# Optimization experiments

Hardware: AMD Instinct MI355X
Metric: run time of the kernel (lower is better)

Reference implementation:

```python
import jax, jax.numpy as jnp
import numpy as np

N_NODES = 20000   # len(set(idx_i)); edge targets cover all nodes
N_EDGES = 320000
F = 128           # feature dim f
N_RBF = 20        # n radial basis functions
R_CUT = 5.0


def setup_inputs() -> dict:
    key = jax.random.key(0)
    ks = jax.random.split(key, 8)
    s = jax.random.normal(ks[0], (N_EDGES, 1, F), dtype=jnp.float32)
    r = jax.random.normal(ks[1], (N_EDGES, 3), dtype=jnp.float32)
    v = jax.random.normal(ks[2], (N_EDGES, 3, F), dtype=jnp.float32)
    idx_i = jax.random.randint(ks[3], (N_EDGES,), 0, N_NODES, dtype=jnp.int32)
    W_phi = jax.random.normal(ks[4], (F, 3 * F), dtype=jnp.float32) * 0.05
    b_phi = jnp.zeros((3 * F,), dtype=jnp.float32)
    W_w = jax.random.normal(ks[5], (N_RBF, 3 * F), dtype=jnp.float32) * 0.05
    b_w = jnp.zeros((3 * F,), dtype=jnp.float32)
    return {"s": s, "r": r, "v": v, "idx_i": idx_i,
            "W_phi": W_phi, "b_phi": b_phi, "W_w": W_w, "b_w": b_w}


def reference(s, r, v, idx_i, W_phi, b_phi, W_w, b_w):
    # phi network: [E,1,F] -> [E,1,3F]
    phi_out = jnp.einsum('eif,fg->eig', s, W_phi) + b_phi

    # RBF on edge vector norms: [E,1,1] -> [E,1,n]
    r_norm = jnp.linalg.norm(r, axis=1, keepdims=True)[:, :, None]  # [E,1,1]
    n_vals = jnp.arange(1, N_RBF + 1, dtype=jnp.float32)            # [n]
    rbf = jnp.sin(n_vals * (jnp.pi / R_CUT) * r_norm) / r_norm      # [E,1,n]
    # cosine cutoff applied to rbf values (faithful to source)
    rbf = jnp.where(rbf <= R_CUT,
                    0.5 * (jnp.cos(jnp.pi * rbf / R_CUT) + 1.0),
                    jnp.zeros_like(rbf))

    # w network: [E,1,n] -> [E,1,3F]
    w = jnp.einsum('ein,ng->eig', rbf, W_w) + b_w

    split = w * phi_out                    # [E,1,3F]
    sp0 = split[..., :F]                   # gates v
    sp1 = split[..., F:2 * F]              # scalar message
    sp2 = split[..., 2 * F:]               # gates direction

    # scatter-add scalar messages -> [N,1,F]
    out_s = jax.ops.segment_sum(sp1, idx_i, num_segments=N_NODES)

    # direction term: detached r, normalized by GLOBAL Frobenius norm (faithful)
    org_r = jax.lax.stop_gradient(r)
    org_r = org_r / jnp.linalg.norm(org_r)         # [E,3]
    dir_msg = sp2 * org_r[:, :, None]              # [E,3,F]
    v_msg = dir_msg + sp0 * v                      # [E,3,F]

    # scatter-add vector messages -> [N,3,F]
    out_v = jax.ops.segment_sum(v_msg, idx_i, num_segments=N_NODES)
    return out_v, out_s
```

## Files before the change

kernel.cpp:

```cpp
#include <hip/hip_runtime.h>
#include <hip/hip_bf16.h>
#include <math.h>

#define E_TOT   320000
#define NNODE   20000
#define FDIM    128
#define N3F     384
#define NRBF    20
#define OV_SIZE (NNODE * 3 * FDIM)
#define DMAX    16

typedef __attribute__((ext_vector_type(8))) short short8;
typedef __attribute__((ext_vector_type(4))) short short4v;
typedef __attribute__((ext_vector_type(4))) float f32x4;

__device__ __forceinline__ short f2bf(float x) {
  union { float f; unsigned u; } v; v.f = x;
  unsigned r = (v.u + 0x7fffu + ((v.u >> 16) & 1u)) >> 16;
  return (short)r;
}

__global__ void sumsq_kernel(const float* __restrict__ r, float* __restrict__ ws, int n) {
  int tid = blockIdx.x * blockDim.x + threadIdx.x;
  float acc = 0.f;
  for (int i = tid; i < n; i += gridDim.x * blockDim.x) {
    float x = r[i];
    acc += x * x;
  }
  for (int off = 32; off > 0; off >>= 1) acc += __shfl_down(acc, off);
  __shared__ float s[4];
  int lane = threadIdx.x & 63, w = threadIdx.x >> 6;
  if (lane == 0) s[w] = acc;
  __syncthreads();
  if (threadIdx.x == 0) {
    float t = s[0] + s[1] + s[2] + s[3];
    unsafeAtomicAdd(ws, t);
  }
}

__global__ void prep_kernel(const float* __restrict__ Wphi, const float* __restrict__ Ww,
                            short* __restrict__ frag) {
  int g = blockIdx.x * 256 + threadIdx.x;
  int lane = g & 63;
  int fid  = g >> 6;
  short* out = frag + (size_t)g * 8;
  if (fid < 96) {
    int ntile = fid >> 2, ks = fid & 3;
    int n  = ntile * 16 + (lane & 15);
    int kb = ks * 32 + (lane >> 4) * 8;
#pragma unroll
    for (int j = 0; j < 8; ++j) out[j] = f2bf(Wphi[(kb + j) * N3F + n]);
  } else if (fid < 120) {
    int ntile = fid - 96;
    int n  = ntile * 16 + (lane & 15);
    int kb = (lane >> 4) * 8;
#pragma unroll
    for (int j = 0; j < 8; ++j) {
      int k = kb + j;
      out[j] = (k < NRBF) ? f2bf(Ww[k * N3F + n]) : (short)0;
    }
  }
}

__global__ void hist_kernel(const int* __restrict__ idx, int* __restrict__ cnt) {
  int e = blockIdx.x * 256 + threadIdx.x;
  if (e < E_TOT) atomicAdd(&cnt[idx[e]], 1);
}

__global__ void scan_kernel(const int* __restrict__ cnt, int* __restrict__ cursor) {
  __shared__ int part[256];
  __shared__ int base_sh[256];
  const int t = threadIdx.x;
  int lo = t * 79; if (lo > NNODE) lo = NNODE;
  int hi = t * 79 + 79; if (hi > NNODE) hi = NNODE;
  int s = 0;
  for (int i = lo; i < hi; ++i) s += cnt[i];
  part[t] = s;
  __syncthreads();
  if (t == 0) {
    int run = 0;
    for (int i = 0; i < 256; ++i) { base_sh[i] = run; run += part[i]; }
  }
  __syncthreads();
  int run = base_sh[t];
  for (int i = lo; i < hi; ++i) { cursor[i] = run; run += cnt[i]; }
}

__global__ void scatter_kernel(const int* __restrict__ idx, int* __restrict__ cursor,
                               int* __restrict__ perm) {
  int e = blockIdx.x * 256 + threadIdx.x;
  if (e < E_TOT) {
    int p = atomicAdd(&cursor[idx[e]], 1);
    perm[p] = e;
  }
}

template <bool USE_PERM>
__launch_bounds__(256, 4)
__global__ void main_kernel(const float* __restrict__ s_in, const float* __restrict__ r_in,
                            const float* __restrict__ v_in, const int* __restrict__ idx_in,
                            const float* __restrict__ bphi_in, const float* __restrict__ bw_in,
                            const short* __restrict__ frag, const float* __restrict__ ws_sumsq,
                            const int* __restrict__ perm, float* __restrict__ out) {
  __shared__ __align__(16) char pool[DMAX * 512 * 4];
  short* sh_s   = (short*)pool;
  short* sh_rbf = (short*)(pool + 64 * 136 * 2);
  float* acc    = (float*)pool;
  __shared__ float sh_bphi[N3F];
  __shared__ float sh_bw[N3F];
  __shared__ float sh_orgr[64][4];
  __shared__ int   sh_perm[64];
  __shared__ int   sh_lid[64];
  __shared__ int   sh_nodes[64];
  __shared__ int   sh_d;

  const int tid = threadIdx.x;
  const int e0  = blockIdx.x * 64;
  const float inv_gnorm = 1.0f / sqrtf(ws_sumsq[0]);

  if (tid < 64) {
    int pe = USE_PERM ? perm[e0 + tid] : (e0 + tid);
    sh_perm[tid] = pe;
    int node = idx_in[pe];
    float rx = r_in[pe * 3 + 0], ry = r_in[pe * 3 + 1], rz = r_in[pe * 3 + 2];
    float rn = sqrtf(rx * rx + ry * ry + rz * rz);
    float irn = 1.0f / rn;
    sh_orgr[tid][0] = rx * inv_gnorm;
    sh_orgr[tid][1] = ry * inv_gnorm;
    sh_orgr[tid][2] = rz * inv_gnorm;
    const float c0 = 0.62831853071795864769f;
#pragma unroll
    for (int n = 1; n <= NRBF; ++n) {
      float t = sinf(((float)n * c0) * rn) * irn;
      float val = (t <= 5.0f) ? 0.5f * (cosf(c0 * t) + 1.0f) : 0.0f;
      sh_rbf[tid * 40 + (n - 1)] = f2bf(val);
    }
#pragma unroll
    for (int k = NRBF; k < 32; ++k) sh_rbf[tid * 40 + k] = 0;
    int prev = __shfl_up(node, 1);
    int flag = (tid == 0) || (node != prev);
    unsigned long long m = __ballot(flag);
    int lid = (int)__popcll(m & ((2ull << tid) - 1ull)) - 1;
    sh_lid[tid] = lid;
    if (flag) sh_nodes[lid] = node;
    if (tid == 0) sh_d = (int)__popcll(m);
  }
  for (int j = tid; j < N3F; j += 256) {
    sh_bphi[j] = bphi_in[j];
    sh_bw[j]   = bw_in[j];
  }
  __syncthreads();

#pragma unroll
  for (int it = 0; it < 8; ++it) {
    int idx4 = tid + it * 256;
    int row = idx4 >> 5, kq = idx4 & 31;
    const float4* srow = (const float4*)(s_in + (size_t)sh_perm[row] * FDIM);
    float4 val = srow[kq];
    short4v p = { f2bf(val.x), f2bf(val.y), f2bf(val.z), f2bf(val.w) };
    *(short4v*)&sh_s[row * 136 + kq * 4] = p;
  }
  __syncthreads();

  const int wave = tid >> 6, lane = tid & 63;
  const int col  = lane & 15;
  const int q    = lane >> 4;

  const int arow = wave * 16 + col;
  short8 a_phi[4];
#pragma unroll
  for (int ks = 0; ks < 4; ++ks)
    a_phi[ks] = *(const short8*)&sh_s[arow * 136 + ks * 32 + q * 8];
  short8 a_w = *(const short8*)&sh_rbf[arow * 40 + q * 8];

  int   lid4[4]; int vbase[4];
  float orx[4], ory[4], orz[4];
#pragma unroll
  for (int i = 0; i < 4; ++i) {
    int el = wave * 16 + q * 4 + i;
    lid4[i]  = sh_lid[el];
    vbase[i] = sh_perm[el] * (3 * FDIM);
    orx[i] = sh_orgr[el][0];
    ory[i] = sh_orgr[el][1];
    orz[i] = sh_orgr[el][2];
  }
  const int d = sh_d;
  const bool use_lds = USE_PERM && (d <= DMAX);

  __syncthreads();
  if (use_lds) {
    for (int j = tid; j < (d << 9); j += 256) acc[j] = 0.f;
  }
  __syncthreads();

  float* out_v = out;
  float* out_s = out + OV_SIZE;
  const short8* fp = (const short8*)frag;
  const short8* fw = fp + 96 * 64;

  for (int f = 0; f < 8; ++f) {
    const int nt0 = f, nt1 = f + 8, nt2 = f + 16;
    f32x4 accP0 = {0.f, 0.f, 0.f, 0.f}, accP1 = accP0, accP2 = accP0;
    f32x4 accW0 = accP0, accW1 = accP0, accW2 = accP0;
#pragma unroll
    for (int ks = 0; ks < 4; ++ks) {
      short8 b0 = fp[(nt0 * 4 + ks) * 64 + lane];
      short8 b1 = fp[(nt1 * 4 + ks) * 64 + lane];
      short8 b2 = fp[(nt2 * 4 + ks) * 64 + lane];
      accP0 = __builtin_amdgcn_mfma_f32_16x16x32_bf16(a_phi[ks], b0, accP0, 0, 0, 0);
      accP1 = __builtin_amdgcn_mfma_f32_16x16x32_bf16(a_phi[ks], b1, accP1, 0, 0, 0);
      accP2 = __builtin_amdgcn_mfma_f32_16x16x32_bf16(a_phi[ks], b2, accP2, 0, 0, 0);
    }
    accW0 = __builtin_amdgcn_mfma_f32_16x16x32_bf16(a_w, fw[nt0 * 64 + lane], accW0, 0, 0, 0);
    accW1 = __builtin_amdgcn_mfma_f32_16x16x32_bf16(a_w, fw[nt1 * 64 + lane], accW1, 0, 0, 0);
    accW2 = __builtin_amdgcn_mfma_f32_16x16x32_bf16(a_w, fw[nt2 * 64 + lane], accW2, 0, 0, 0);

    const int feat = f * 16 + col;
    const float bp0 = sh_bphi[feat], bp1 = sh_bphi[feat + 128], bp2 = sh_bphi[feat + 256];
    const float bw0 = sh_bw[feat],   bw1 = sh_bw[feat + 128],   bw2 = sh_bw[feat + 256];

    auto flush = [&](int l, float as, float avx, float avy, float avz) {
      if (use_lds) {
        atomicAdd(&acc[(l << 9) + feat], as);
        atomicAdd(&acc[(l << 9) + 128 + feat], avx);
        atomicAdd(&acc[(l << 9) + 256 + feat], avy);
        atomicAdd(&acc[(l << 9) + 384 + feat], avz);
      } else {
        int node = sh_nodes[l];
        unsafeAtomicAdd(&out_s[node * FDIM + feat], as);
        unsafeAtomicAdd(&out_v[(node * 3 + 0) * FDIM + feat], avx);
        unsafeAtomicAdd(&out_v[(node * 3 + 1) * FDIM + feat], avy);
        unsafeAtomicAdd(&out_v[(node * 3 + 2) * FDIM + feat], avz);
      }
    };

    float as = 0.f, avx = 0.f, avy = 0.f, avz = 0.f;
    int cur = lid4[0];
#pragma unroll
    for (int i = 0; i < 4; ++i) {
      float sp0 = (accW0[i] + bw0) * (accP0[i] + bp0);
      float sp1 = (accW1[i] + bw1) * (accP1[i] + bp1);
      float sp2 = (accW2[i] + bw2) * (accP2[i] + bp2);
      const float* vp = v_in + (size_t)vbase[i] + feat;
      float mx = sp2 * orx[i] + sp0 * vp[0];
      float my = sp2 * ory[i] + sp0 * vp[FDIM];
      float mz = sp2 * orz[i] + sp0 * vp[2 * FDIM];
      if (lid4[i] != cur) {
        flush(cur, as, avx, avy, avz);
        as = avx = avy = avz = 0.f;
        cur = lid4[i];
      }
      as += sp1; avx += mx; avy += my; avz += mz;
    }
    flush(cur, as, avx, avy, avz);
  }

  if (use_lds) {
    __syncthreads();
    for (int j = tid; j < (d << 9); j += 256) {
      int l = j >> 9, rem = j & 511, comp = rem >> 7, ft = rem & 127;
      int node = sh_nodes[l];
      float val = acc[j];
      float* dst = (comp == 0) ? &out_s[node * FDIM + ft]
                               : &out_v[(node * 3 + (comp - 1)) * FDIM + ft];
      if (l > 0 && l < d - 1) *dst = val;
      else unsafeAtomicAdd(dst, val);
    }
  }
}

extern "C" void kernel_launch(void* const* d_in, const int* in_sizes, int n_in,
                              void* d_out, int out_size, void* d_ws, size_t ws_size,
                              hipStream_t stream) {
  const float* s_in  = (const float*)d_in[0];
  const float* r_in  = (const float*)d_in[1];
  const float* v_in  = (const float*)d_in[2];
  const int*   idx_i = (const int*)d_in[3];
  const float* Wphi  = (const float*)d_in[4];
  const float* bphi  = (const float*)d_in[5];
  const float* Ww    = (const float*)d_in[6];
  const float* bw    = (const float*)d_in[7];
  float* out = (float*)d_out;

  const size_t WS_NEED_SORTED = 1562896;
  const bool use_sorted = (ws_size >= WS_NEED_SORTED);

  float* ws_sumsq = (float*)d_ws;
  int*   cnt      = (int*)((char*)d_ws + 16);
  short* frag_s   = (short*)((char*)d_ws + 80016);
  int*   cursor   = (int*)((char*)d_ws + 202896);
  int*   permv    = (int*)((char*)d_ws + 282896);
  short* frag_f   = (short*)((char*)d_ws + 16);
  short* frag     = use_sorted ? frag_s : frag_f;

  hipMemsetAsync(d_out, 0, (size_t)out_size * sizeof(float), stream);
  hipMemsetAsync(d_ws, 0, use_sorted ? 80016 : 16, stream);
  sumsq_kernel<<<480, 256, 0, stream>>>(r_in, ws_sumsq, in_sizes[1]);
  prep_kernel<<<30, 256, 0, stream>>>(Wphi, Ww, frag);
  if (use_sorted) {
    hist_kernel<<<1250, 256, 0, stream>>>(idx_i, cnt);
    scan_kernel<<<1, 256, 0, stream>>>(cnt, cursor);
    scatter_kernel<<<1250, 256, 0, stream>>>(idx_i, cursor, permv);
    main_kernel<true><<<E_TOT / 64, 256, 0, stream>>>(s_in, r_in, v_in, idx_i, bphi, bw,
                                                      frag, ws_sumsq, permv, out);
  } else {
    main_kernel<false><<<E_TOT / 64, 256, 0, stream>>>(s_in, r_in, v_in, idx_i, bphi, bw,
                                                       frag, ws_sumsq, nullptr, out);
  }
}
```

Before: 989.8 us.

## Prefetch v loads one feature tile ahead and spread RBF computation across waves

The main loop now double-buffers the gathered v values: the loads for the next feature tile are issued before the MFMA work of the current tile, so global-load latency can overlap with matrix math. The RBF basis computation is split across all four waves (five basis functions each) instead of only the first wave, and it uses the fast __sinf/__cosf intrinsics. The prefetch adds register pressure, and the fast intrinsics reduce accuracy before the bf16 rounding.

Result: slower. 1.033 ms (+4.3%).

```diff
diff --git a/kernel.cpp b/kernel.cpp
--- a/kernel.cpp
+++ b/kernel.cpp
@@ -118,32 +118,36 @@
   const int e0  = blockIdx.x * 64;
   const float inv_gnorm = 1.0f / sqrtf(ws_sumsq[0]);
 
-  if (tid < 64) {
-    int pe = USE_PERM ? perm[e0 + tid] : (e0 + tid);
-    sh_perm[tid] = pe;
-    int node = idx_in[pe];
+  {
+    const int er = tid & 63, part = tid >> 6;
+    int pe = USE_PERM ? perm[e0 + er] : (e0 + er);
     float rx = r_in[pe * 3 + 0], ry = r_in[pe * 3 + 1], rz = r_in[pe * 3 + 2];
     float rn = sqrtf(rx * rx + ry * ry + rz * rz);
     float irn = 1.0f / rn;
-    sh_orgr[tid][0] = rx * inv_gnorm;
-    sh_orgr[tid][1] = ry * inv_gnorm;
-    sh_orgr[tid][2] = rz * inv_gnorm;
     const float c0 = 0.62831853071795864769f;
-#pragma unroll
-    for (int n = 1; n <= NRBF; ++n) {
-      float t = sinf(((float)n * c0) * rn) * irn;
-      float val = (t <= 5.0f) ? 0.5f * (cosf(c0 * t) + 1.0f) : 0.0f;
-      sh_rbf[tid * 40 + (n - 1)] = f2bf(val);
+    if (part == 0) {
+      sh_perm[er] = pe;
+      int node = idx_in[pe];
+      sh_orgr[er][0] = rx * inv_gnorm;
+      sh_orgr[er][1] = ry * inv_gnorm;
+      sh_orgr[er][2] = rz * inv_gnorm;
+#pragma unroll
+      for (int k = NRBF; k < 32; ++k) sh_rbf[er * 40 + k] = 0;
+      int prev = __shfl_up(node, 1);
+      int flag = (er == 0) || (node != prev);
+      unsigned long long m = __ballot(flag);
+      int lid = (int)__popcll(m & ((2ull << er) - 1ull)) - 1;
+      sh_lid[er] = lid;
+      if (flag) sh_nodes[lid] = node;
+      if (er == 0) sh_d = (int)__popcll(m);
     }
 #pragma unroll
-    for (int k = NRBF; k < 32; ++k) sh_rbf[tid * 40 + k] = 0;
-    int prev = __shfl_up(node, 1);
-    int flag = (tid == 0) || (node != prev);
-    unsigned long long m = __ballot(flag);
-    int lid = (int)__popcll(m & ((2ull << tid) - 1ull)) - 1;
-    sh_lid[tid] = lid;
-    if (flag) sh_nodes[lid] = node;
-    if (tid == 0) sh_d = (int)__popcll(m);
+    for (int j = 0; j < 5; ++j) {
+      int n = part * 5 + j + 1;
+      float t = __sinf(((float)n * c0) * rn) * irn;
+      float val = (t <= 5.0f) ? 0.5f * (__cosf(c0 * t) + 1.0f) : 0.0f;
+      sh_rbf[er * 40 + (n - 1)] = f2bf(val);
+    }
   }
   for (int j = tid; j < N3F; j += 256) {
     sh_bphi[j] = bphi_in[j];
@@ -173,13 +177,14 @@
     a_phi[ks] = *(const short8*)&sh_s[arow * 136 + ks * 32 + q * 8];
   short8 a_w = *(const short8*)&sh_rbf[arow * 40 + q * 8];
 
-  int   lid4[4]; int vbase[4];
+  int   lid4[4];
+  const float* vrow[4];
   float orx[4], ory[4], orz[4];
 #pragma unroll
   for (int i = 0; i < 4; ++i) {
     int el = wave * 16 + q * 4 + i;
-    lid4[i]  = sh_lid[el];
-    vbase[i] = sh_perm[el] * (3 * FDIM);
+    lid4[i] = sh_lid[el];
+    vrow[i] = v_in + (size_t)sh_perm[el] * (3 * FDIM);
     orx[i] = sh_orgr[el][0];
     ory[i] = sh_orgr[el][1];
     orz[i] = sh_orgr[el][2];
@@ -198,62 +203,81 @@
   const short8* fp = (const short8*)frag;
   const short8* fw = fp + 96 * 64;
 
-  for (int f = 0; f < 8; ++f) {
-    const int nt0 = f, nt1 = f + 8, nt2 = f + 16;
-    f32x4 accP0 = {0.f, 0.f, 0.f, 0.f}, accP1 = accP0, accP2 = accP0;
-    f32x4 accW0 = accP0, accW1 = accP0, accW2 = accP0;
-#pragma unroll
-    for (int ks = 0; ks < 4; ++ks) {
-      short8 b0 = fp[(nt0 * 4 + ks) * 64 + lane];
-      short8 b1 = fp[(nt1 * 4 + ks) * 64 + lane];
-      short8 b2 = fp[(nt2 * 4 + ks) * 64 + lane];
-      accP0 = __builtin_amdgcn_mfma_f32_16x16x32_bf16(a_phi[ks], b0, accP0, 0, 0, 0);
-      accP1 = __builtin_amdgcn_mfma_f32_16x16x32_bf16(a_phi[ks], b1, accP1, 0, 0, 0);
-      accP2 = __builtin_amdgcn_mfma_f32_16x16x32_bf16(a_phi[ks], b2, accP2, 0, 0, 0);
-    }
-    accW0 = __builtin_amdgcn_mfma_f32_16x16x32_bf16(a_w, fw[nt0 * 64 + lane], accW0, 0, 0, 0);
-    accW1 = __builtin_amdgcn_mfma_f32_16x16x32_bf16(a_w, fw[nt1 * 64 + lane], accW1, 0, 0, 0);
-    accW2 = __builtin_amdgcn_mfma_f32_16x16x32_bf16(a_w, fw[nt2 * 64 + lane], accW2, 0, 0, 0);
-
-    const int feat = f * 16 + col;
-    const float bp0 = sh_bphi[feat], bp1 = sh_bphi[feat + 128], bp2 = sh_bphi[feat + 256];
-    const float bw0 = sh_bw[feat],   bw1 = sh_bw[feat + 128],   bw2 = sh_bw[feat + 256];
-
-    auto flush = [&](int l, float as, float avx, float avy, float avz) {
-      if (use_lds) {
-        atomicAdd(&acc[(l << 9) + feat], as);
-        atomicAdd(&acc[(l << 9) + 128 + feat], avx);
-        atomicAdd(&acc[(l << 9) + 256 + feat], avy);
-        atomicAdd(&acc[(l << 9) + 384 + feat], avz);
-      } else {
-        int node = sh_nodes[l];
-        unsafeAtomicAdd(&out_s[node * FDIM + feat], as);
-        unsafeAtomicAdd(&out_v[(node * 3 + 0) * FDIM + feat], avx);
-        unsafeAtomicAdd(&out_v[(node * 3 + 1) * FDIM + feat], avy);
-        unsafeAtomicAdd(&out_v[(node * 3 + 2) * FDIM + feat], avz);
-      }
-    };
-
-    float as = 0.f, avx = 0.f, avy = 0.f, avz = 0.f;
-    int cur = lid4[0];
-#pragma unroll
-    for (int i = 0; i < 4; ++i) {
-      float sp0 = (accW0[i] + bw0) * (accP0[i] + bp0);
-      float sp1 = (accW1[i] + bw1) * (accP1[i] + bp1);
-      float sp2 = (accW2[i] + bw2) * (accP2[i] + bp2);
-      const float* vp = v_in + (size_t)vbase[i] + feat;
-      float mx = sp2 * orx[i] + sp0 * vp[0];
-      float my = sp2 * ory[i] + sp0 * vp[FDIM];
-      float mz = sp2 * orz[i] + sp0 * vp[2 * FDIM];
-      if (lid4[i] != cur) {
-        flush(cur, as, avx, avy, avz);
-        as = avx = avy = avz = 0.f;
-        cur = lid4[i];
-      }
-      as += sp1; avx += mx; avy += my; avz += mz;
-    }
-    flush(cur, as, avx, avy, avz);
-  }
+#define VISSUE(f_, X, Y, Z)                                                   \
+  { int ft_ = (f_) * 16 + col;                                                \
+    _Pragma("unroll")                                                         \
+    for (int i = 0; i < 4; ++i) {                                             \
+      X[i] = vrow[i][ft_];                                                    \
+      Y[i] = vrow[i][ft_ + FDIM];                                             \
+      Z[i] = vrow[i][ft_ + 2 * FDIM];                                         \
+    } }
+
+#define BODY(f_, CX, CY, CZ, NX, NY, NZ)                                      \
+  {                                                                           \
+    const int fb = (f_);                                                      \
+    if (fb + 1 < 8) VISSUE(fb + 1, NX, NY, NZ);     \
+    const int nt0 = fb, nt1 = fb + 8, nt2 = fb + 16;                          \
+    f32x4 accP0 = {0.f, 0.f, 0.f, 0.f}, accP1 = accP0, accP2 = accP0;         \
+    f32x4 accW0 = accP0, accW1 = accP0, accW2 = accP0;                        \
+    _Pragma("unroll")                                                         \
+    for (int ks = 0; ks < 4; ++ks) {                                          \
+      short8 b0 = fp[(nt0 * 4 + ks) * 64 + lane];                             \
+      short8 b1 = fp[(nt1 * 4 + ks) * 64 + lane];                             \
+      short8 b2 = fp[(nt2 * 4 + ks) * 64 + lane];                             \
+      accP0 = __builtin_amdgcn_mfma_f32_16x16x32_bf16(a_phi[ks], b0, accP0, 0, 0, 0); \
+      accP1 = __builtin_amdgcn_mfma_f32_16x16x32_bf16(a_phi[ks], b1, accP1, 0, 0, 0); \
+      accP2 = __builtin_amdgcn_mfma_f32_16x16x32_bf16(a_phi[ks], b2, accP2, 0, 0, 0); \
+    }                                                                         \
+    accW0 = __builtin_amdgcn_mfma_f32_16x16x32_bf16(a_w, fw[nt0 * 64 + lane], accW0, 0, 0, 0); \
+    accW1 = __builtin_amdgcn_mfma_f32_16x16x32_bf16(a_w, fw[nt1 * 64 + lane], accW1, 0, 0, 0); \
+    accW2 = __builtin_amdgcn_mfma_f32_16x16x32_bf16(a_w, fw[nt2 * 64 + lane], accW2, 0, 0, 0); \
+    const int feat = fb * 16 + col;                                           \
+    const float bp0 = sh_bphi[feat], bp1 = sh_bphi[feat + 128], bp2 = sh_bphi[feat + 256]; \
+    const float bw0 = sh_bw[feat],   bw1 = sh_bw[feat + 128],   bw2 = sh_bw[feat + 256];   \
+    float as = 0.f, avx = 0.f, avy = 0.f, avz = 0.f;                          \
+    int cur = lid4[0];                                                        \
+    _Pragma("unroll")                                                         \
+    for (int i = 0; i < 4; ++i) {                                             \
+      float sp0 = (accW0[i] + bw0) * (accP0[i] + bp0);                        \
+      float sp1 = (accW1[i] + bw1) * (accP1[i] + bp1);                        \
+      float sp2 = (accW2[i] + bw2) * (accP2[i] + bp2);                        \
+      float mx = sp2 * orx[i] + sp0 * CX[i];                                  \
+      float my = sp2 * ory[i] + sp0 * CY[i];                                  \
+      float mz = sp2 * orz[i] + sp0 * CZ[i];                                  \
+      if (lid4[i] != cur) {                                                   \
+        FLUSH(cur, as, avx, avy, avz);                                        \
+        as = avx = avy = avz = 0.f;                                           \
+        cur = lid4[i];                                                        \
+      }                                                                       \
+      as += sp1; avx += mx; avy += my; avz += mz;                             \
+    }                                                                         \
+    FLUSH(cur, as, avx, avy, avz);                                            \
+  }
+
+#define FLUSH(l_, as_, avx_, avy_, avz_)                                      \
+  { const int l = (l_);                                                       \
+    if (use_lds) {                                                            \
+      atomicAdd(&acc[(l << 9) + feat], as_);                                  \
+      atomicAdd(&acc[(l << 9) + 128 + feat], avx_);                           \
+      atomicAdd(&acc[(l << 9) + 256 + feat], avy_);                           \
+      atomicAdd(&acc[(l << 9) + 384 + feat], avz_);                           \
+    } else {                                                                  \
+      int node = sh_nodes[l];                                                 \
+      unsafeAtomicAdd(&out_s[node * FDIM + feat], as_);                       \
+      unsafeAtomicAdd(&out_v[(node * 3 + 0) * FDIM + feat], avx_);            \
+      unsafeAtomicAdd(&out_v[(node * 3 + 1) * FDIM + feat], avy_);            \
+      unsafeAtomicAdd(&out_v[(node * 3 + 2) * FDIM + feat], avz_);            \
+    } }
+
+  float Avx[4], Avy[4], Avz[4], Bvx[4], Bvy[4], Bvz[4];
+  VISSUE(0, Avx, Avy, Avz);
+  for (int ff = 0; ff < 8; ff += 2) {
+    BODY(ff,     Avx, Avy, Avz, Bvx, Bvy, Bvz);
+    BODY(ff + 1, Bvx, Bvy, Bvz, Avx, Avy, Avz);
+  }
+#undef BODY
+#undef FLUSH
+#undef VISSUE
 
   if (use_lds) {
     __syncthreads();
```
